# Performance work log

Hardware: AMD Instinct MI355X
Metric: run time of the kernel (lower is better)

The kernel has to match this reference:

```python
import jax, jax.numpy as jnp
import numpy as np


def setup_inputs() -> dict:
    key = jax.random.key(0)
    k1, k2 = jax.random.split(key)
    # light field: [B, U(angular), H, W, V(angular)]
    lfi = jax.random.normal(k1, (4, 9, 256, 256, 9), dtype=jnp.float32)
    # center-view feature maps: [B, H, W, n_filters]; positive values so the
    # height normalization (divide by per-map max) is well defined.
    f_maps = jax.random.uniform(k2, (4, 256, 256, 64), dtype=jnp.float32)
    return {"lfi": lfi, "f_maps": f_maps}


def reference(lfi, f_maps):
    # relative_size: sum of each [H,W] feature map -> [B, N]
    s_mask = jnp.sum(f_maps, axis=(1, 2))
    # height: mean over rows (axis H) -> [B, W, N]; normalize each map's
    # height vector by its max; rearrange to [B, N, W]
    hv = jnp.mean(f_maps, axis=1)
    hv = hv / jnp.max(hv, axis=1, keepdims=True)
    h_mask = jnp.transpose(hv, (0, 2, 1))  # [B, N, W] (== [B, N, H], h == w)

    # Original loop computes, per (b, n):
    #   combined[b,n,u,y,x,v] = lfi[b,u,y,x,v] * s_mask[b,n] * h_mask[b,n,y]
    # then mean over v (axis 5) and transpose to [B, U, Y, X, N].
    # The per-(b,n) scaling is independent of v, so it commutes with the mean.
    mean_lfi = jnp.mean(lfi, axis=4)  # [B, U, Y, X]
    out = jnp.einsum('buyx,bn,bny->buyxn', mean_lfi, s_mask, h_mask)
    return out
```

## Files before the change

### kernel.cpp

```cpp
#include <hip/hip_runtime.h>

#define BB 4
#define UU 9
#define HH 256
#define WW 256
#define VV 9
#define NF 64
#define NPIX (BB * UU * HH * WW)

typedef float f32x4 __attribute__((ext_vector_type(4)));

__global__ __launch_bounds__(256) void k_hv(const float* __restrict__ f,
                                            float* __restrict__ hv) {
    const int blk = blockIdx.x;
    const int b = blk >> 8, w = blk & 255;
    const int t = threadIdx.x;
    const int n = t & 63, hc = t >> 6;

    float acc = 0.f;
    const float* p = f + (((size_t)(b * HH + hc * 64) * WW) + w) * NF + n;
    const size_t stride = (size_t)WW * NF;
    #pragma unroll 8
    for (int i = 0; i < 64; ++i) acc += p[(size_t)i * stride];

    __shared__ float red[4][64];
    red[hc][n] = acc;
    __syncthreads();
    if (t < 64) {
        float s = red[0][t] + red[1][t] + red[2][t] + red[3][t];
        hv[((size_t)b * WW + w) * NF + t] = s * (1.0f / HH);
    }
}

__global__ __launch_bounds__(256) void k_comb(const float* __restrict__ hv,
                                              float* __restrict__ comb) {
    const int b = blockIdx.x;
    const int t = threadIdx.x;
    const int n = t & 63, c = t >> 6;

    float s = 0.f, m = -1e30f;
    const float* p = hv + ((size_t)b * WW + c * 64) * NF + n;
    #pragma unroll 8
    for (int i = 0; i < 64; ++i) {
        float v = p[(size_t)i * NF];
        s += v;
        m = fmaxf(m, v);
    }

    __shared__ float rs[4][64], rm[4][64];
    __shared__ float fscale[64];
    rs[c][n] = s;
    rm[c][n] = m;
    __syncthreads();
    if (t < 64) {
        float ssum = (rs[0][t] + rs[1][t] + rs[2][t] + rs[3][t]) * (float)HH;
        float smax = fmaxf(fmaxf(rm[0][t], rm[1][t]), fmaxf(rm[2][t], rm[3][t]));
        fscale[t] = ssum / smax;
    }
    __syncthreads();

    const float sc = fscale[n];
    const float* p2 = hv + ((size_t)b * WW + c * 64) * NF + n;
    float* q = comb + ((size_t)b * WW + c * 64) * NF + n;
    #pragma unroll 8
    for (int i = 0; i < 64; ++i) q[(size_t)i * NF] = p2[(size_t)i * NF] * sc;
}

__global__ __launch_bounds__(256) void k_mean(const float* __restrict__ lfi,
                                              float* __restrict__ mlfi) {
    const int pix = blockIdx.x * 256 + threadIdx.x;
    const float* lp = lfi + (size_t)pix * VV;
    float s = lp[0] + lp[1] + lp[2] + lp[3] + lp[4]
            + lp[5] + lp[6] + lp[7] + lp[8];
    mlfi[pix] = s * (1.0f / VV);
}

__global__ __launch_bounds__(256) void k_out(const float* __restrict__ mlfi,
                                             const float* __restrict__ comb,
                                             float* __restrict__ out) {
    const int wid  = (int)((blockIdx.x * 256 + threadIdx.x) >> 6);
    const int lane = threadIdx.x & 63;
    const int y  = wid & 255;
    const int b  = (wid >> 8) / UU;

    const int q   = lane & 15;
    const int sub = lane >> 4;

    const size_t rowpix = (size_t)wid * 256;
    const f32x4 c4 = *(const f32x4*)(comb + ((size_t)(b * 256 + y)) * NF + q * 4);

    #pragma unroll 8
    for (int g = 0; g < 64; ++g) {
        const size_t pix = rowpix + (size_t)g * 4 + sub;
        const float m = mlfi[pix];
        f32x4 o = c4 * m;
        __builtin_nontemporal_store(o, (f32x4*)(out + pix * NF + (size_t)q * 4));
    }
}

extern "C" void kernel_launch(void* const* d_in, const int* in_sizes, int n_in,
                              void* d_out, int out_size, void* d_ws, size_t ws_size,
                              hipStream_t stream) {
    const float* lfi    = (const float*)d_in[0];
    const float* f_maps = (const float*)d_in[1];
    float* out = (float*)d_out;

    float* hv   = (float*)d_ws;
    float* comb = hv + (size_t)BB * WW * NF;
    float* mlfi = comb + (size_t)BB * WW * NF;

    k_hv<<<BB * WW, 256, 0, stream>>>(f_maps, hv);
    k_comb<<<BB, 256, 0, stream>>>(hv, comb);
    k_mean<<<NPIX / 256, 256, 0, stream>>>(lfi, mlfi);
    k_out<<<(BB * UU * HH) / 4, 256, 0, stream>>>(mlfi, comb, out);
}
```

Before: 145.7 us.

## Fuse light-field angular mean into output kernel via shared-memory staging

```diff
diff --git a/kernel.cpp b/kernel.cpp
--- a/kernel.cpp
+++ b/kernel.cpp
@@ -6,7 +6,8 @@
 #define WW 256
 #define VV 9
 #define NF 64
-#define NPIX (BB * UU * HH * WW)
+#define NROWS (BB * UU * HH)
+#define ROWS 4
 
 typedef float f32x4 __attribute__((ext_vector_type(4)));
 
@@ -66,35 +67,49 @@
     for (int i = 0; i < 64; ++i) q[(size_t)i * NF] = p2[(size_t)i * NF] * sc;
 }
 
-__global__ __launch_bounds__(256) void k_mean(const float* __restrict__ lfi,
-                                              float* __restrict__ mlfi) {
-    const int pix = blockIdx.x * 256 + threadIdx.x;
-    const float* lp = lfi + (size_t)pix * VV;
-    float s = lp[0] + lp[1] + lp[2] + lp[3] + lp[4]
-            + lp[5] + lp[6] + lp[7] + lp[8];
-    mlfi[pix] = s * (1.0f / VV);
-}
-
-__global__ __launch_bounds__(256) void k_out(const float* __restrict__ mlfi,
+__global__ __launch_bounds__(256) void k_out(const float* __restrict__ lfi,
                                              const float* __restrict__ comb,
                                              float* __restrict__ out) {
-    const int wid  = (int)((blockIdx.x * 256 + threadIdx.x) >> 6);
-    const int lane = threadIdx.x & 63;
-    const int y  = wid & 255;
-    const int b  = (wid >> 8) / UU;
+    __shared__ float slfi[ROWS * WW * VV];
+    __shared__ float smean[ROWS * WW];
+
+    const int blk = blockIdx.x;
+    const int t = threadIdx.x;
+
+    const f32x4* src = (const f32x4*)(lfi + (size_t)blk * (ROWS * WW * VV));
+    f32x4* dst = (f32x4*)slfi;
+    #pragma unroll
+    for (int j = 0; j < 9; ++j) dst[t + 256 * j] = src[t + 256 * j];
+    __syncthreads();
+
+    #pragma unroll
+    for (int j = 0; j < ROWS; ++j) {
+        const int p = t + 256 * j;
+        const float* lp = slfi + p * VV;
+        float s = lp[0] + lp[1] + lp[2] + lp[3] + lp[4]
+                + lp[5] + lp[6] + lp[7] + lp[8];
+        smean[p] = s * (1.0f / VV);
+    }
+    __syncthreads();
+
+    const int lane = t & 63, w = t >> 6;
+    const int rowid = blk * ROWS + w;
+    const int y = rowid & 255;
+    const int b = (rowid >> 8) / UU;
 
     const int q   = lane & 15;
     const int sub = lane >> 4;
 
-    const size_t rowpix = (size_t)wid * 256;
-    const f32x4 c4 = *(const f32x4*)(comb + ((size_t)(b * 256 + y)) * NF + q * 4);
+    const f32x4 c4 = *(const f32x4*)(comb + ((size_t)(b * WW + y)) * NF + q * 4);
+    float* obase = out + (size_t)rowid * WW * NF + (size_t)q * 4;
+    const float* mbase = smean + w * WW;
 
     #pragma unroll 8
     for (int g = 0; g < 64; ++g) {
-        const size_t pix = rowpix + (size_t)g * 4 + sub;
-        const float m = mlfi[pix];
+        const int pl = g * 4 + sub;
+        const float m = mbase[pl];
         f32x4 o = c4 * m;
-        __builtin_nontemporal_store(o, (f32x4*)(out + pix * NF + (size_t)q * 4));
+        __builtin_nontemporal_store(o, (f32x4*)(obase + (size_t)pl * NF));
     }
 }
 
@@ -107,10 +122,8 @@
 
     float* hv   = (float*)d_ws;
     float* comb = hv + (size_t)BB * WW * NF;
-    float* mlfi = comb + (size_t)BB * WW * NF;
 
     k_hv<<<BB * WW, 256, 0, stream>>>(f_maps, hv);
     k_comb<<<BB, 256, 0, stream>>>(hv, comb);
-    k_mean<<<NPIX / 256, 256, 0, stream>>>(lfi, mlfi);
-    k_out<<<(BB * UU * HH) / 4, 256, 0, stream>>>(mlfi, comb, out);
+    k_out<<<NROWS / ROWS, 256, 0, stream>>>(lfi, comb, out);
 }
```

New measurement: 128.0 us. 12.2% less time.
